# Kernel optimization log

Hardware: AMD Instinct MI355X
Metric: run time of the kernel (lower is better)

Reference implementation:

```python
import jax, jax.numpy as jnp
from jax import lax
import numpy as np

NPOINT, RADIUS, NSAMPLE = 512, 0.2, 32
BN_EPS = 1e-5


def _index_points(points, idx):
    # points: [B, N, C]; idx: [B, ...] int -> [B, ..., C]
    return jax.vmap(lambda p, i: p[i])(points, idx)


def _farthest_point_sample(xyz, npoint):
    # xyz: [B, N, 3] -> [B, npoint] int32 (deterministic start at index 0)
    B, N, _ = xyz.shape
    def step(carry, _):
        distance, farthest = carry  # [B,N], [B]
        centroid = xyz[jnp.arange(B), farthest]            # [B,3]
        d = jnp.sum((xyz - centroid[:, None, :]) ** 2, -1)  # [B,N]
        distance = jnp.minimum(distance, d)
        nxt = jnp.argmax(distance, axis=-1).astype(jnp.int32)
        return (distance, nxt), farthest
    init = (jnp.full((B, N), 1e10, xyz.dtype), jnp.zeros((B,), jnp.int32))
    _, idxs = lax.scan(step, init, None, length=npoint)
    return idxs.T  # [B, npoint]


def _query_ball_point(radius, nsample, xyz, new_xyz):
    # xyz: [B,N,3], new_xyz: [B,S,3] -> [B,S,nsample] int32
    B, N, _ = xyz.shape
    S = new_xyz.shape[1]
    # squared distances [B,S,N]
    sqrdists = (jnp.sum(new_xyz ** 2, -1)[:, :, None]
                + jnp.sum(xyz ** 2, -1)[:, None, :]
                - 2.0 * jnp.einsum('bsc,bnc->bsn', new_xyz, xyz))
    group_idx = jnp.broadcast_to(jnp.arange(N, dtype=jnp.int32), (B, S, N))
    group_idx = jnp.where(sqrdists > radius * radius, N, group_idx)
    group_idx = jnp.sort(group_idx, axis=-1)[:, :, :nsample]
    first = group_idx[:, :, :1]
    return jnp.where(group_idx == N, first, group_idx)


def _mlp_layer(x, w, b, g, be):
    # x: [B, Cin, K, S]; 1x1 conv + BatchNorm2d (training stats) + relu
    y = jnp.einsum('bcks,oc->boks', x, w) + b[None, :, None, None]
    mean = jnp.mean(y, axis=(0, 2, 3), keepdims=True)
    var = jnp.mean((y - mean) ** 2, axis=(0, 2, 3), keepdims=True)
    y = (y - mean) * lax.rsqrt(var + BN_EPS)
    y = y * g[None, :, None, None] + be[None, :, None, None]
    return jax.nn.relu(y)


def setup_inputs() -> dict:
    key = jax.random.key(0)
    ks = jax.random.split(key, 16)
    inp = {
        'xyz': jax.random.uniform(ks[0], (8, 3, 16384), jnp.float32),
        'points': jax.random.normal(ks[1], (8, 3, 16384), jnp.float32),
    }
    chans = [6, 64, 64, 128]
    for i in range(3):
        cin, cout = chans[i], chans[i + 1]
        inp[f'w{i}'] = jax.random.normal(ks[2 + 4 * i], (cout, cin), jnp.float32) / np.float32(np.sqrt(cin))
        inp[f'b{i}'] = jax.random.normal(ks[3 + 4 * i], (cout,), jnp.float32) * 0.01
        inp[f'g{i}'] = jnp.ones((cout,), jnp.float32)
        inp[f'be{i}'] = jnp.zeros((cout,), jnp.float32)
    return inp


def reference(xyz, points, w0, b0, g0, be0, w1, b1, g1, be1, w2, b2, g2, be2):
    xyz_t = jnp.transpose(xyz, (0, 2, 1))      # [B,N,3]
    pts_t = jnp.transpose(points, (0, 2, 1))   # [B,N,D]
    B, N, C = xyz_t.shape

    fps_idx = _farthest_point_sample(xyz_t, NPOINT)        # [B,S]
    new_xyz = _index_points(xyz_t, fps_idx)                # [B,S,3]
    group_idx = _query_ball_point(RADIUS, NSAMPLE, xyz_t, new_xyz)  # [B,S,K]
    grouped_xyz = _index_points(xyz_t, group_idx) - new_xyz[:, :, None, :]  # [B,S,K,3]
    grouped_pts = _index_points(pts_t, group_idx)          # [B,S,K,D]
    new_points = jnp.concatenate([grouped_pts, grouped_xyz], axis=-1)  # [B,S,K,D+3]

    x = jnp.transpose(new_points, (0, 3, 2, 1))  # [B, C, K, S]
    for (w, b, g, be) in ((w0, b0, g0, be0), (w1, b1, g1, be1), (w2, b2, g2, be2)):
        x = _mlp_layer(x, w, b, g, be)
    new_feat = jnp.max(x, axis=2)                # [B, 128, S]
    new_xyz_out = jnp.transpose(new_xyz, (0, 2, 1))  # [B, 3, S]
    return (new_xyz_out, new_feat)
```

## Files before the change

### kernel.cpp

```cpp
#include <hip/hip_runtime.h>
#include <cstdint>
#include <cstddef>

#define BB 8
#define NN 16384
#define SS 512
#define KK 32

__device__ __forceinline__ float fm(float a, float b){ return __fmul_rn(a,b); }
__device__ __forceinline__ float fa(float a, float b){ return __fadd_rn(a,b); }
__device__ __forceinline__ float fsb(float a, float b){ return __fsub_rn(a,b); }

__global__ __launch_bounds__(1024, 4) void fps_kernel(const float* __restrict__ xyz,
                                                      float* __restrict__ nxyz,
                                                      float* __restrict__ out)
{
  int b = blockIdx.x;
  int t = threadIdx.x;
  const float* xb = xyz + (size_t)b*3*NN;
  float px[16], py[16], pz[16], dist[16];
#pragma unroll
  for (int k=0;k<16;k++){
    int n = k*1024 + t;
    px[k]=xb[n]; py[k]=xb[NN+n]; pz[k]=xb[2*NN+n];
    dist[k]=1e10f;
  }
#pragma unroll
  for (int k=0;k<16;k++){
    asm volatile("" : "+v"(px[k]), "+v"(py[k]), "+v"(pz[k]));
  }
  __shared__ unsigned long long redk[2][16];
  int wid = t >> 6, lane = t & 63;
  float cx = xb[0], cy = xb[NN], cz = xb[2*NN];
  for (int step=0; step<SS; ++step){
    if (t==0){
      float* nx = nxyz + ((size_t)b*SS + step)*3;
      nx[0]=cx; nx[1]=cy; nx[2]=cz;
      float* ox = out + (size_t)b*3*SS;
      ox[step]=cx; ox[SS+step]=cy; ox[2*SS+step]=cz;
    }
    float bv = -1.0f; int bk = 0;
#pragma unroll
    for (int k=0;k<16;k++){
      float dx=fsb(px[k],cx), dy=fsb(py[k],cy), dz=fsb(pz[k],cz);
      float d = fa(fa(fm(dx,dx),fm(dy,dy)),fm(dz,dz));
      float dk = fminf(dist[k], d);
      dist[k]=dk;
      if (dk > bv){ bv=dk; bk=k; }
    }
    int bi = (bk<<10) | t;
    unsigned long long key = ((unsigned long long)__float_as_uint(bv) << 32)
                           | (unsigned)(16384 - bi);
#pragma unroll
    for (int off=1; off<64; off<<=1){
      unsigned long long ok = __shfl_xor(key, off);
      if (ok > key) key = ok;
    }
    int par = step & 1;
    if (lane==0) redk[par][wid] = key;
    __syncthreads();
    unsigned long long k2 = redk[par][lane & 15];
#pragma unroll
    for (int off=1; off<16; off<<=1){
      unsigned long long ok = __shfl_xor(k2, off);
      if (ok > k2) k2 = ok;
    }
    int i = 16384 - (int)(unsigned)(k2 & 0xFFFFFFFFull);
    cx = xb[i]; cy = xb[NN+i]; cz = xb[2*NN+i];
  }
}

__global__ void ballq_kernel(const float* __restrict__ xyz,
                             const float* __restrict__ nxyz,
                             int* __restrict__ gidx)
{
  int wv = (blockIdx.x * (blockDim.x>>6)) + (threadIdx.x>>6);
  int lane = threadIdx.x & 63;
  int b = wv >> 9; int s = wv & (SS-1);
  const float* nx3 = nxyz + ((size_t)b*SS + s)*3;
  float nx=nx3[0], ny=nx3[1], nz=nx3[2];
  float cn = fa(fa(fm(nx,nx),fm(ny,ny)),fm(nz,nz));
  const float* xb = xyz + (size_t)b*3*NN;
  const float R2 = (float)(0.2*0.2);
  int* g = gidx + ((size_t)b*SS + s)*KK;
  int cnt = 0; int first_idx = 0;
  for (int base=0; base<NN; base+=64){
    int n = base + lane;
    float x=xb[n], y=xb[NN+n], z=xb[2*NN+n];
    float sq = fa(fa(fm(x,x),fm(y,y)),fm(z,z));
    float dot = fa(fa(fm(nx,x),fm(ny,y)),fm(nz,z));
    float sqd = fsb(fa(cn, sq), fm(2.0f, dot));
    bool inb = !(sqd > R2);
    unsigned long long m = __ballot(inb);
    if (m){
      if (cnt==0) first_idx = base + __builtin_ctzll(m);
      int pre = __popcll(m & ((1ull<<lane)-1ull));
      int slot = cnt + pre;
      if (inb && slot < KK) g[slot] = n;
      cnt += __popcll(m);
      if (cnt >= KK) break;
    }
  }
  if (cnt < KK && lane >= cnt && lane < KK) g[lane] = first_idx;
}

__global__ __launch_bounds__(256) void mlp0_kernel(const float* __restrict__ xyz,
                            const float* __restrict__ pts,
                            const float* __restrict__ nxyz,
                            const int* __restrict__ gidx,
                            const float* __restrict__ w,
                            const float* __restrict__ bias,
                            float* __restrict__ y0)
{
  int gid = blockIdx.x*blockDim.x + threadIdx.x;
  int b = gid / (KK*SS);
  int r = gid % (KK*SS);
  int k = r / SS; int s = r % SS;
  int idx = gidx[((size_t)b*SS + s)*KK + k];
  const float* pb = pts + (size_t)b*3*NN;
  const float* xb = xyz + (size_t)b*3*NN;
  const float* nx3 = nxyz + ((size_t)b*SS + s)*3;
  float in[6];
  in[0]=pb[idx]; in[1]=pb[NN+idx]; in[2]=pb[2*NN+idx];
  in[3]=xb[idx]-nx3[0]; in[4]=xb[NN+idx]-nx3[1]; in[5]=xb[2*NN+idx]-nx3[2];
  float* po = y0 + (size_t)b*64*KK*SS + r;
  for (int o=0;o<64;o++){
    float acc = bias[o];
#pragma unroll
    for (int c=0;c<6;c++) acc += in[c]*w[o*6+c];
    po[(size_t)o*KK*SS] = acc;
  }
}

__global__ __launch_bounds__(256) void stats_part_kernel(const float* __restrict__ y, int C,
                                                         double* __restrict__ psum)
{
  int o = blockIdx.x >> 3; int b = blockIdx.x & 7;
  int t = threadIdx.x;
  const float4* p = (const float4*)(y + ((size_t)b*C + o)*KK*SS);
  double s1=0.0, s2=0.0;
#pragma unroll
  for (int i=0;i<16;i++){
    float4 v = p[t + i*256];
    double x0=v.x, x1=v.y, x2=v.z, x3=v.w;
    s1 += x0+x1; s1 += x2+x3;
    s2 += x0*x0 + x1*x1;
    s2 += x2*x2 + x3*x3;
  }
#pragma unroll
  for (int off=32; off>=1; off>>=1){
    s1 += __shfl_down(s1, off);
    s2 += __shfl_down(s2, off);
  }
  __shared__ double l1[4], l2[4];
  int wid = t>>6;
  if ((t&63)==0){ l1[wid]=s1; l2[wid]=s2; }
  __syncthreads();
  if (t==0){
    double t1=l1[0]+l1[1]+l1[2]+l1[3];
    double t2=l2[0]+l2[1]+l2[2]+l2[3];
    psum[(o*8+b)*2+0]=t1;
    psum[(o*8+b)*2+1]=t2;
  }
}

template<int C>
__device__ __forceinline__ void bn_finalize_lds(const double* __restrict__ psum,
                                                const float* __restrict__ gamma,
                                                const float* __restrict__ beta,
                                                float* sa, float* sc)
{
  int o = threadIdx.x;
  if (o < C){
    double t1=0.0, t2=0.0;
#pragma unroll
    for (int b=0;b<8;b++){ t1 += psum[(o*8+b)*2+0]; t2 += psum[(o*8+b)*2+1]; }
    double n = (double)BB*KK*SS;
    double m = t1/n;
    double var = t2/n - m*m;
    double inv = 1.0/sqrt(var + 1e-5);
    float s = (float)((double)gamma[o]*inv);
    sa[o]=s; sc[o]=(float)((double)beta[o] - m*(double)s);
  }
  __syncthreads();
}

template<int CIN, int COUT>
__global__ __launch_bounds__(256) void mlp_kernel(const float* __restrict__ yin,
                            const float* __restrict__ w,
                            const float* __restrict__ bias,
                            const double* __restrict__ psum,
                            const float* __restrict__ gamma,
                            const float* __restrict__ beta,
                            float* __restrict__ yout)
{
  __shared__ float sa[CIN], sc[CIN];
  bn_finalize_lds<CIN>(psum, gamma, beta, sa, sc);
  int gid = blockIdx.x*blockDim.x + threadIdx.x;
  int b = gid / (KK*SS);
  int r = gid % (KK*SS);
  const float* pin = yin + (size_t)b*CIN*KK*SS + r;
  float x[CIN];
#pragma unroll
  for (int ci=0;ci<CIN;ci++) x[ci] = fmaxf(fmaf(pin[(size_t)ci*KK*SS], sa[ci], sc[ci]), 0.0f);
  float* po = yout + (size_t)b*COUT*KK*SS + r;
  for (int o=0;o<COUT;o++){
    float acc = bias[o];
#pragma unroll
    for (int ci=0;ci<CIN;ci++) acc += x[ci]*w[o*CIN+ci];
    po[(size_t)o*KK*SS] = acc;
  }
}

__global__ __launch_bounds__(256) void final_kernel(const float* __restrict__ y2,
                             const double* __restrict__ psum,
                             const float* __restrict__ gamma,
                             const float* __restrict__ beta,
                             float* __restrict__ out)
{
  __shared__ float sa[128], sc[128];
  bn_finalize_lds<128>(psum, gamma, beta, sa, sc);
  int gid = blockIdx.x*blockDim.x + threadIdx.x;
  int b = gid / (128*128);
  int r = gid % (128*128);
  int o = r >> 7; int s4 = (r & 127);
  const float4* p = (const float4*)(y2 + ((size_t)b*128 + o)*KK*SS) + s4;
  float scv=sa[o], sh=sc[o];
  float m0=0.f,m1=0.f,m2=0.f,m3=0.f;
#pragma unroll
  for (int k=0;k<KK;k++){
    float4 v = p[k*(SS/4)];
    m0 = fmaxf(m0, fmaxf(fmaf(v.x, scv, sh), 0.0f));
    m1 = fmaxf(m1, fmaxf(fmaf(v.y, scv, sh), 0.0f));
    m2 = fmaxf(m2, fmaxf(fmaf(v.z, scv, sh), 0.0f));
    m3 = fmaxf(m3, fmaxf(fmaf(v.w, scv, sh), 0.0f));
  }
  float4* po = (float4*)(out + ((size_t)b*128 + o)*SS) + s4;
  *po = make_float4(m0,m1,m2,m3);
}

extern "C" void kernel_launch(void* const* d_in, const int* in_sizes, int n_in,
                              void* d_out, int out_size, void* d_ws, size_t ws_size,
                              hipStream_t stream)
{
  const float* xyz = (const float*)d_in[0];
  const float* pts = (const float*)d_in[1];
  const float* w0  = (const float*)d_in[2];
  const float* b0  = (const float*)d_in[3];
  const float* g0  = (const float*)d_in[4];
  const float* be0 = (const float*)d_in[5];
  const float* w1  = (const float*)d_in[6];
  const float* b1  = (const float*)d_in[7];
  const float* g1  = (const float*)d_in[8];
  const float* be1 = (const float*)d_in[9];
  const float* w2  = (const float*)d_in[10];
  const float* b2  = (const float*)d_in[11];
  const float* g2  = (const float*)d_in[12];
  const float* be2 = (const float*)d_in[13];
  float* out = (float*)d_out;

  char* ws = (char*)d_ws;
  float*  nxyz = (float*) (ws + 524288);
  int*    gidx = (int*)   (ws + 573440);
  double* ps0  = (double*)(ws + 1099776);
  double* ps1  = (double*)(ws + 1107968);
  double* ps2  = (double*)(ws + 1116160);
  float* y1 = (float*)(ws + 4194304);
  float* y2 = (float*)(ws + 41943040);
  float* y0 = (float*)(ws + 79691776);
  (void)ws_size; (void)in_sizes; (void)n_in; (void)out_size;

  fps_kernel<<<dim3(BB), dim3(1024), 0, stream>>>(xyz, nxyz, out);
  ballq_kernel<<<dim3(1024), dim3(256), 0, stream>>>(xyz, nxyz, gidx);
  mlp0_kernel<<<dim3(512), dim3(256), 0, stream>>>(xyz, pts, nxyz, gidx, w0, b0, y0);
  stats_part_kernel<<<dim3(64*8), dim3(256), 0, stream>>>(y0, 64, ps0);
  mlp_kernel<64,64><<<dim3(512), dim3(256), 0, stream>>>(y0, w1, b1, ps0, g0, be0, y1);
  stats_part_kernel<<<dim3(64*8), dim3(256), 0, stream>>>(y1, 64, ps1);
  mlp_kernel<64,128><<<dim3(512), dim3(256), 0, stream>>>(y1, w2, b2, ps1, g1, be1, y2);
  stats_part_kernel<<<dim3(128*8), dim3(256), 0, stream>>>(y2, 128, ps2);
  final_kernel<<<dim3(512), dim3(256), 0, stream>>>(y2, ps2, g2, be2, out + BB*3*SS);
}
```

Baseline: 1.296 ms.

## Fuse ball query, MLP and BN stats stages into one persistent kernel with grid barriers

Replaces eight separate launches after farthest-point sampling with a single persistent kernel of 512 blocks that runs each stage in turn, separated by atomic-counter grid barriers. The barrier counter is reset inside the FPS kernel. This removes per-launch overhead and tail gaps between stages. It relies on all 512 blocks being co-resident, and the barriers add spin-wait costs.

New measurement: 1.980 ms. 1.53x slower.

```diff
diff --git a/kernel.cpp b/kernel.cpp
--- a/kernel.cpp
+++ b/kernel.cpp
@@ -6,6 +6,7 @@
 #define NN 16384
 #define SS 512
 #define KK 32
+#define NB 512
 
 __device__ __forceinline__ float fm(float a, float b){ return __fmul_rn(a,b); }
 __device__ __forceinline__ float fa(float a, float b){ return __fadd_rn(a,b); }
@@ -13,8 +14,12 @@
 
 __global__ __launch_bounds__(1024, 4) void fps_kernel(const float* __restrict__ xyz,
                                                       float* __restrict__ nxyz,
-                                                      float* __restrict__ out)
-{
+                                                      float* __restrict__ out,
+                                                      unsigned* __restrict__ bar)
+{
+  if (blockIdx.x==0 && threadIdx.x<2){
+    __hip_atomic_store(&bar[threadIdx.x], 0u, __ATOMIC_RELAXED, __HIP_MEMORY_SCOPE_AGENT);
+  }
   int b = blockIdx.x;
   int t = threadIdx.x;
   const float* xb = xyz + (size_t)b*3*NN;
@@ -70,11 +75,29 @@
   }
 }
 
-__global__ void ballq_kernel(const float* __restrict__ xyz,
-                             const float* __restrict__ nxyz,
-                             int* __restrict__ gidx)
-{
-  int wv = (blockIdx.x * (blockDim.x>>6)) + (threadIdx.x>>6);
+__device__ __forceinline__ void gridbar(unsigned* __restrict__ bar, unsigned phase){
+  __syncthreads();
+  if (threadIdx.x == 0){
+    __builtin_amdgcn_fence(__ATOMIC_RELEASE, "agent");
+    unsigned old = __hip_atomic_fetch_add(&bar[0], 1u, __ATOMIC_ACQ_REL, __HIP_MEMORY_SCOPE_AGENT);
+    if (old == (unsigned)(NB-1)){
+      __hip_atomic_store(&bar[0], 0u, __ATOMIC_RELAXED, __HIP_MEMORY_SCOPE_AGENT);
+      __hip_atomic_store(&bar[1], phase, __ATOMIC_RELEASE, __HIP_MEMORY_SCOPE_AGENT);
+    }
+  }
+  if (threadIdx.x < 64){
+    while (__hip_atomic_load(&bar[1], __ATOMIC_ACQUIRE, __HIP_MEMORY_SCOPE_AGENT) < phase){
+      __builtin_amdgcn_s_sleep(2);
+    }
+  }
+  __syncthreads();
+  __builtin_amdgcn_fence(__ATOMIC_ACQUIRE, "agent");
+}
+
+
+__device__ __forceinline__ void ballq_one(const float* __restrict__ xyz,
+                                          const float* __restrict__ nxyz,
+                                          int* __restrict__ gidx, int wv){
   int lane = threadIdx.x & 63;
   int b = wv >> 9; int s = wv & (SS-1);
   const float* nx3 = nxyz + ((size_t)b*SS + s)*3;
@@ -104,38 +127,9 @@
   if (cnt < KK && lane >= cnt && lane < KK) g[lane] = first_idx;
 }
 
-__global__ __launch_bounds__(256) void mlp0_kernel(const float* __restrict__ xyz,
-                            const float* __restrict__ pts,
-                            const float* __restrict__ nxyz,
-                            const int* __restrict__ gidx,
-                            const float* __restrict__ w,
-                            const float* __restrict__ bias,
-                            float* __restrict__ y0)
-{
-  int gid = blockIdx.x*blockDim.x + threadIdx.x;
-  int b = gid / (KK*SS);
-  int r = gid % (KK*SS);
-  int k = r / SS; int s = r % SS;
-  int idx = gidx[((size_t)b*SS + s)*KK + k];
-  const float* pb = pts + (size_t)b*3*NN;
-  const float* xb = xyz + (size_t)b*3*NN;
-  const float* nx3 = nxyz + ((size_t)b*SS + s)*3;
-  float in[6];
-  in[0]=pb[idx]; in[1]=pb[NN+idx]; in[2]=pb[2*NN+idx];
-  in[3]=xb[idx]-nx3[0]; in[4]=xb[NN+idx]-nx3[1]; in[5]=xb[2*NN+idx]-nx3[2];
-  float* po = y0 + (size_t)b*64*KK*SS + r;
-  for (int o=0;o<64;o++){
-    float acc = bias[o];
-#pragma unroll
-    for (int c=0;c<6;c++) acc += in[c]*w[o*6+c];
-    po[(size_t)o*KK*SS] = acc;
-  }
-}
-
-__global__ __launch_bounds__(256) void stats_part_kernel(const float* __restrict__ y, int C,
-                                                         double* __restrict__ psum)
-{
-  int o = blockIdx.x >> 3; int b = blockIdx.x & 7;
+__device__ __forceinline__ void stats_one(const float* __restrict__ y, int C,
+                                          double* __restrict__ psum, int vb){
+  int o = vb >> 3; int b = vb & 7;
   int t = threadIdx.x;
   const float4* p = (const float4*)(y + ((size_t)b*C + o)*KK*SS);
   double s1=0.0, s2=0.0;
@@ -162,6 +156,7 @@
     psum[(o*8+b)*2+0]=t1;
     psum[(o*8+b)*2+1]=t2;
   }
+  __syncthreads();
 }
 
 template<int C>
@@ -186,13 +181,13 @@
 }
 
 template<int CIN, int COUT>
-__global__ __launch_bounds__(256) void mlp_kernel(const float* __restrict__ yin,
-                            const float* __restrict__ w,
-                            const float* __restrict__ bias,
-                            const double* __restrict__ psum,
-                            const float* __restrict__ gamma,
-                            const float* __restrict__ beta,
-                            float* __restrict__ yout)
+__device__ __forceinline__ void mlp_one(const float* __restrict__ yin,
+                                        const float* __restrict__ w,
+                                        const float* __restrict__ bias,
+                                        const double* __restrict__ psum,
+                                        const float* __restrict__ gamma,
+                                        const float* __restrict__ beta,
+                                        float* __restrict__ yout)
 {
   __shared__ float sa[CIN], sc[CIN];
   bn_finalize_lds<CIN>(psum, gamma, beta, sa, sc);
@@ -210,33 +205,92 @@
     for (int ci=0;ci<CIN;ci++) acc += x[ci]*w[o*CIN+ci];
     po[(size_t)o*KK*SS] = acc;
   }
-}
-
-__global__ __launch_bounds__(256) void final_kernel(const float* __restrict__ y2,
-                             const double* __restrict__ psum,
-                             const float* __restrict__ gamma,
-                             const float* __restrict__ beta,
-                             float* __restrict__ out)
-{
-  __shared__ float sa[128], sc[128];
-  bn_finalize_lds<128>(psum, gamma, beta, sa, sc);
-  int gid = blockIdx.x*blockDim.x + threadIdx.x;
-  int b = gid / (128*128);
-  int r = gid % (128*128);
-  int o = r >> 7; int s4 = (r & 127);
-  const float4* p = (const float4*)(y2 + ((size_t)b*128 + o)*KK*SS) + s4;
-  float scv=sa[o], sh=sc[o];
-  float m0=0.f,m1=0.f,m2=0.f,m3=0.f;
-#pragma unroll
-  for (int k=0;k<KK;k++){
-    float4 v = p[k*(SS/4)];
-    m0 = fmaxf(m0, fmaxf(fmaf(v.x, scv, sh), 0.0f));
-    m1 = fmaxf(m1, fmaxf(fmaf(v.y, scv, sh), 0.0f));
-    m2 = fmaxf(m2, fmaxf(fmaf(v.z, scv, sh), 0.0f));
-    m3 = fmaxf(m3, fmaxf(fmaf(v.w, scv, sh), 0.0f));
-  }
-  float4* po = (float4*)(out + ((size_t)b*128 + o)*SS) + s4;
-  *po = make_float4(m0,m1,m2,m3);
+  __syncthreads();
+}
+
+__global__ __launch_bounds__(256, 2) void mega_kernel(const float* __restrict__ xyz,
+                            const float* __restrict__ pts,
+                            const float* __restrict__ nxyz,
+                            int* __restrict__ gidx,
+                            const float* __restrict__ w0, const float* __restrict__ b0,
+                            const float* __restrict__ g0, const float* __restrict__ be0,
+                            const float* __restrict__ w1, const float* __restrict__ b1,
+                            const float* __restrict__ g1, const float* __restrict__ be1,
+                            const float* __restrict__ w2, const float* __restrict__ b2,
+                            const float* __restrict__ g2, const float* __restrict__ be2,
+                            float* __restrict__ y0, float* __restrict__ y1, float* __restrict__ y2,
+                            double* __restrict__ ps0, double* __restrict__ ps1, double* __restrict__ ps2,
+                            float* __restrict__ out,
+                            unsigned* __restrict__ bar)
+{
+  const int bid = blockIdx.x, tid = threadIdx.x;
+
+  {
+    int wv0 = (bid*4 + (tid>>6))*2;
+    ballq_one(xyz, nxyz, gidx, wv0);
+    ballq_one(xyz, nxyz, gidx, wv0+1);
+  }
+  gridbar(bar, 1);
+
+  {
+    int gid = bid*256 + tid;
+    int b = gid / (KK*SS);
+    int r = gid % (KK*SS);
+    int k = r / SS; int s = r % SS;
+    int idx = gidx[((size_t)b*SS + s)*KK + k];
+    const float* pb = pts + (size_t)b*3*NN;
+    const float* xb = xyz + (size_t)b*3*NN;
+    const float* nx3 = nxyz + ((size_t)b*SS + s)*3;
+    float in[6];
+    in[0]=pb[idx]; in[1]=pb[NN+idx]; in[2]=pb[2*NN+idx];
+    in[3]=xb[idx]-nx3[0]; in[4]=xb[NN+idx]-nx3[1]; in[5]=xb[2*NN+idx]-nx3[2];
+    float* po = y0 + (size_t)b*64*KK*SS + r;
+    for (int o=0;o<64;o++){
+      float acc = b0[o];
+#pragma unroll
+      for (int c=0;c<6;c++) acc += in[c]*w0[o*6+c];
+      po[(size_t)o*KK*SS] = acc;
+    }
+  }
+  gridbar(bar, 2);
+
+  stats_one(y0, 64, ps0, bid);
+  gridbar(bar, 3);
+
+  mlp_one<64,64>(y0, w1, b1, ps0, g0, be0, y1);
+  gridbar(bar, 4);
+
+  stats_one(y1, 64, ps1, bid);
+  gridbar(bar, 5);
+
+  mlp_one<64,128>(y1, w2, b2, ps1, g1, be1, y2);
+  gridbar(bar, 6);
+
+  stats_one(y2, 128, ps2, bid);
+  stats_one(y2, 128, ps2, bid + NB);
+  gridbar(bar, 7);
+
+  {
+    __shared__ float sa[128], sc[128];
+    bn_finalize_lds<128>(ps2, g2, be2, sa, sc);
+    int gid = bid*256 + tid;
+    int b = gid / (128*128);
+    int r = gid % (128*128);
+    int o = r >> 7; int s4 = (r & 127);
+    const float4* p = (const float4*)(y2 + ((size_t)b*128 + o)*KK*SS) + s4;
+    float scv=sa[o], sh=sc[o];
+    float m0=0.f,m1=0.f,m2=0.f,m3=0.f;
+#pragma unroll
+    for (int k=0;k<KK;k++){
+      float4 v = p[k*(SS/4)];
+      m0 = fmaxf(m0, fmaxf(fmaf(v.x, scv, sh), 0.0f));
+      m1 = fmaxf(m1, fmaxf(fmaf(v.y, scv, sh), 0.0f));
+      m2 = fmaxf(m2, fmaxf(fmaf(v.z, scv, sh), 0.0f));
+      m3 = fmaxf(m3, fmaxf(fmaf(v.w, scv, sh), 0.0f));
+    }
+    float4* po = (float4*)(out + ((size_t)b*128 + o)*SS) + s4;
+    *po = make_float4(m0,m1,m2,m3);
+  }
 }
 
 extern "C" void kernel_launch(void* const* d_in, const int* in_sizes, int n_in,
@@ -265,18 +319,14 @@
   double* ps0  = (double*)(ws + 1099776);
   double* ps1  = (double*)(ws + 1107968);
   double* ps2  = (double*)(ws + 1116160);
+  unsigned* bar = (unsigned*)(ws + 1132544);
   float* y1 = (float*)(ws + 4194304);
   float* y2 = (float*)(ws + 41943040);
   float* y0 = (float*)(ws + 79691776);
   (void)ws_size; (void)in_sizes; (void)n_in; (void)out_size;
 
-  fps_kernel<<<dim3(BB), dim3(1024), 0, stream>>>(xyz, nxyz, out);
-  ballq_kernel<<<dim3(1024), dim3(256), 0, stream>>>(xyz, nxyz, gidx);
-  mlp0_kernel<<<dim3(512), dim3(256), 0, stream>>>(xyz, pts, nxyz, gidx, w0, b0, y0);
-  stats_part_kernel<<<dim3(64*8), dim3(256), 0, stream>>>(y0, 64, ps0);
-  mlp_kernel<64,64><<<dim3(512), dim3(256), 0, stream>>>(y0, w1, b1, ps0, g0, be0, y1);
-  stats_part_kernel<<<dim3(64*8), dim3(256), 0, stream>>>(y1, 64, ps1);
-  mlp_kernel<64,128><<<dim3(512), dim3(256), 0, stream>>>(y1, w2, b2, ps1, g1, be1, y2);
-  stats_part_kernel<<<dim3(128*8), dim3(256), 0, stream>>>(y2, 128, ps2);
-  final_kernel<<<dim3(512), dim3(256), 0, stream>>>(y2, ps2, g2, be2, out + BB*3*SS);
-}
+  fps_kernel<<<dim3(BB), dim3(1024), 0, stream>>>(xyz, nxyz, out, bar);
+  mega_kernel<<<dim3(NB), dim3(256), 0, stream>>>(xyz, pts, nxyz, gidx,
+      w0, b0, g0, be0, w1, b1, g1, be1, w2, b2, g2, be2,
+      y0, y1, y2, ps0, ps1, ps2, out + BB*3*SS, bar);
+}
```
